# Kernel optimization log

Measured on AMD Instinct MI355X. Metric: run time of the kernel, lower is better.

## Reference

```python
import jax, jax.numpy as jnp
import numpy as np

SEQ_LEN = 2048
DIM = 1024
HEADS = 16
DIM_HEAD = 64
INNER = HEADS * DIM_HEAD
BASE = 10000.0


def rope_tables(seq_len, head_dim):
    inv_freq = 1.0 / (BASE ** (jnp.arange(0, head_dim, 2, dtype=jnp.float32) / head_dim))
    t = jnp.arange(seq_len, dtype=jnp.float32)
    freqs = jnp.einsum('i,j->ij', t, inv_freq)          # [n, d/2]
    emb = jnp.concatenate([freqs, freqs], axis=-1)       # [n, d]
    return jnp.cos(emb), jnp.sin(emb)                    # each [n, d]


def rotate_half(x):
    d = x.shape[-1] // 2
    return jnp.concatenate([-x[..., d:], x[..., :d]], axis=-1)


def setup_inputs() -> dict:
    key = jax.random.key(0)
    ks = jax.random.split(key, 5)
    x = jax.random.normal(ks[0], (2, SEQ_LEN, DIM), dtype=jnp.float32)
    W_qkv = jax.random.normal(ks[1], (DIM, 3 * INNER), dtype=jnp.float32) * (DIM ** -0.5)
    W_out = jax.random.normal(ks[2], (INNER, DIM), dtype=jnp.float32) * (INNER ** -0.5)
    b_out = jnp.zeros((DIM,), dtype=jnp.float32)
    ln_g = jnp.ones((DIM,), dtype=jnp.float32)
    ln_b = jnp.zeros((DIM,), dtype=jnp.float32)
    return {"x": x, "W_qkv": W_qkv, "W_out": W_out, "b_out": b_out, "ln_g": ln_g, "ln_b": ln_b}


def reference(x, W_qkv, W_out, b_out, ln_g, ln_b):
    b, n, _ = x.shape
    # LayerNorm
    mu = jnp.mean(x, axis=-1, keepdims=True)
    var = jnp.mean(jnp.square(x - mu), axis=-1, keepdims=True)
    xn = (x - mu) * jax.lax.rsqrt(var + 1e-5) * ln_g + ln_b
    # QKV projection -> [b, h, n, d]
    qkv = xn @ W_qkv                                   # [b, n, 3*inner]
    q, k, v = jnp.split(qkv, 3, axis=-1)
    def to_heads(t):
        return t.reshape(b, n, HEADS, DIM_HEAD).transpose(0, 2, 1, 3)
    q, k, v = to_heads(q), to_heads(k), to_heads(v)
    # RoPE
    cos, sin = rope_tables(n, DIM_HEAD)                # [n, d]
    cos = cos[None, None]                              # [1,1,n,d]
    sin = sin[None, None]
    q = q * cos + rotate_half(q) * sin
    k = k * cos + rotate_half(k) * sin
    # Attention
    scale = DIM_HEAD ** -0.5
    dots = jnp.einsum('bhid,bhjd->bhij', q, k) * scale  # [b,h,n,n]
    causal = jnp.tril(jnp.ones((n, n), dtype=bool))
    dots = jnp.where(causal[None, None], dots, jnp.float32(-jnp.inf))
    attn = jax.nn.softmax(dots, axis=-1)
    out = jnp.einsum('bhij,bhjd->bhid', attn, v)       # [b,h,n,d]
    out = out.transpose(0, 2, 1, 3).reshape(b, n, INNER)
    return out @ W_out + b_out
```

## Files before the change

kernel.cpp:

```cpp
#include <hip/hip_runtime.h>
#include <hip/hip_bf16.h>

#define SEQ    2048
#define DMODEL 1024
#define HEADS  16
#define DHEAD  64
#define BATCH  2
#define TOK    (BATCH * SEQ)
#define NQKV   (3 * DMODEL)
#define QK_SCALE (0.125f * 1.4426950408889634f)

typedef __attribute__((ext_vector_type(8))) short bf16x8;
typedef __attribute__((ext_vector_type(4))) float f32x4;

__device__ __forceinline__ float bf2f(ushort u) {
  union { unsigned int i; float f; } v; v.i = ((unsigned int)u) << 16; return v.f;
}
__device__ __forceinline__ ushort f2bf(float f) {
  union { float f; unsigned int i; } v; v.f = f;
  unsigned int r = (v.i + 0x7fffu + ((v.i >> 16) & 1u)) >> 16;
  return (ushort)r;
}

__device__ __forceinline__ int swz(int row, int byteoff) {
  return row * 128 + (byteoff ^ ((row & 7) << 4));
}
__device__ __forceinline__ int kperm(int s) {
  return (s & 0x20) | ((s & 0x0C) << 1) | ((s & 0x10) >> 2) | (s & 3);
}

#define GLL16(g, l)                                                                     \
  __builtin_amdgcn_global_load_lds((const __attribute__((address_space(1))) void*)(g),  \
                                   (__attribute__((address_space(3))) void*)(l), 16, 0, 0)

__global__ __launch_bounds__(256) void ln_kernel(const float* __restrict__ x,
                                                 const float* __restrict__ g,
                                                 const float* __restrict__ b,
                                                 ushort* __restrict__ xn) {
  int t = blockIdx.x;
  int tid = threadIdx.x;
  const float* row = x + (size_t)t * DMODEL;
  float4 v = *(const float4*)(row + tid * 4);
  float s  = v.x + v.y + v.z + v.w;
  float s2 = v.x * v.x + v.y * v.y + v.z * v.z + v.w * v.w;
#pragma unroll
  for (int m = 32; m >= 1; m >>= 1) {
    s  += __shfl_down(s, m);
    s2 += __shfl_down(s2, m);
  }
  __shared__ float ws[4], ws2[4];
  if ((tid & 63) == 0) { ws[tid >> 6] = s; ws2[tid >> 6] = s2; }
  __syncthreads();
  s  = ws[0] + ws[1] + ws[2] + ws[3];
  s2 = ws2[0] + ws2[1] + ws2[2] + ws2[3];
  float mu  = s * (1.f / DMODEL);
  float var = s2 * (1.f / DMODEL) - mu * mu;
  float rs  = rsqrtf(var + 1e-5f);
  float4 gv = *(const float4*)(g + tid * 4);
  float4 bv = *(const float4*)(b + tid * 4);
  ushort4 o;
  o.x = f2bf((v.x - mu) * rs * gv.x + bv.x);
  o.y = f2bf((v.y - mu) * rs * gv.y + bv.y);
  o.z = f2bf((v.z - mu) * rs * gv.z + bv.z);
  o.w = f2bf((v.w - mu) * rs * gv.w + bv.w);
  *(ushort4*)(xn + (size_t)t * DMODEL + tid * 4) = o;
}

__global__ void transpose_f2b(const float* __restrict__ in, ushort* __restrict__ out,
                              int R, int C) {
  __shared__ float tile[32][33];
  int c0 = blockIdx.x * 32, r0 = blockIdx.y * 32;
  int x = threadIdx.x, y = threadIdx.y;
#pragma unroll
  for (int i = 0; i < 32; i += 8) tile[y + i][x] = in[(size_t)(r0 + y + i) * C + c0 + x];
  __syncthreads();
#pragma unroll
  for (int i = 0; i < 32; i += 8) out[(size_t)(c0 + y + i) * R + r0 + x] = f2bf(tile[x][y + i]);
}

__global__ void rope_tab_kernel(float* __restrict__ ct, float* __restrict__ st) {
  int n = blockIdx.x, d = threadIdx.x;
  float invf = expf(-logf(10000.f) * (float)(d & 31) * (1.f / 32.f));
  float a = (float)n * invf;
  ct[n * DHEAD + d] = cosf(a);
  st[n * DHEAD + d] = sinf(a);
}

template<int EPI>
__global__ __launch_bounds__(256) void gemm_bt(const ushort* __restrict__ A,
                                               const ushort* __restrict__ BT,
                                               float* __restrict__ Cf,
                                               const float* __restrict__ bias,
                                               ushort* __restrict__ qh,
                                               ushort* __restrict__ kh,
                                               ushort* __restrict__ vh,
                                               const float* __restrict__ ct,
                                               const float* __restrict__ st,
                                               int M, int N, int K) {
  __shared__ __align__(16) ushort As[128 * 32];
  __shared__ __align__(16) ushort Bs[128 * 32];
  int tid = threadIdx.x;
  int w = tid >> 6, lane = tid & 63;
  int lrow = lane & 15, g = lane >> 4;
  int m0 = blockIdx.y * 128, n0 = blockIdx.x * 128;
  int wr = (w >> 1) * 64, wc = (w & 1) * 64;
  int grow = lane >> 2;
  int gcol = ((lane & 3) ^ ((grow >> 1) & 3)) * 8;
  ushort* ldsA0 = As + w * 512;
  ushort* ldsA1 = As + 2048 + w * 512;
  ushort* ldsB0 = Bs + w * 512;
  ushort* ldsB1 = Bs + 2048 + w * 512;
  int fcol = (g ^ ((lrow >> 1) & 3)) * 8;
  f32x4 acc[4][4] = {};
  for (int k0 = 0; k0 < K; k0 += 32) {
    __syncthreads();
    GLL16(A  + (size_t)(m0 + w * 16 + grow) * K + k0 + gcol, ldsA0);
    GLL16(A  + (size_t)(m0 + 64 + w * 16 + grow) * K + k0 + gcol, ldsA1);
    GLL16(BT + (size_t)(n0 + w * 16 + grow) * K + k0 + gcol, ldsB0);
    GLL16(BT + (size_t)(n0 + 64 + w * 16 + grow) * K + k0 + gcol, ldsB1);
    __syncthreads();
    bf16x8 af[4], bfr[4];
#pragma unroll
    for (int i = 0; i < 4; i++) af[i]  = *(const bf16x8*)(As + (wr + i * 16 + lrow) * 32 + fcol);
#pragma unroll
    for (int i = 0; i < 4; i++) bfr[i] = *(const bf16x8*)(Bs + (wc + i * 16 + lrow) * 32 + fcol);
    __builtin_amdgcn_s_setprio(1);
#pragma unroll
    for (int mf = 0; mf < 4; mf++)
#pragma unroll
      for (int nf = 0; nf < 4; nf++)
        acc[mf][nf] = __builtin_amdgcn_mfma_f32_16x16x32_bf16(af[mf], bfr[nf], acc[mf][nf], 0, 0, 0);
    __builtin_amdgcn_s_setprio(0);
  }
#pragma unroll
  for (int mf = 0; mf < 4; mf++)
#pragma unroll
    for (int nf = 0; nf < 4; nf++) {
      int col = n0 + wc + nf * 16 + lrow;
#pragma unroll
      for (int r = 0; r < 4; r++) {
        int rowi = m0 + wr + mf * 16 + g * 4 + r;
        float val = acc[mf][nf][r];
        if (EPI == 2) {
          Cf[(size_t)rowi * N + col] = val + bias[col];
        } else {
          int mat = col >> 10, c1 = col & 1023;
          int h = c1 >> 6, d = c1 & 63;
          int bb = rowi >> 11, n = rowi & (SEQ - 1);
          if (mat < 2) {
            float partner = acc[mf][nf ^ 2][r];
            float cs = ct[n * DHEAD + d], sn = st[n * DHEAD + d];
            float sgn = (d & 32) ? 1.f : -1.f;
            val = val * cs + sgn * partner * sn;
            if (mat == 0) val *= QK_SCALE;
          }
          ushort* dst = (mat == 0) ? qh : (mat == 1) ? kh : vh;
          dst[((size_t)(bb * HEADS + h) * SEQ + n) * DHEAD + d] = f2bf(val);
        }
      }
    }
}

__global__ __launch_bounds__(256) void attn_kernel(const ushort* __restrict__ q,
                                                   const ushort* __restrict__ k,
                                                   const ushort* __restrict__ v,
                                                   ushort* __restrict__ ao) {
  int wgid = blockIdx.x + gridDim.x * blockIdx.y;
  int j5 = wgid >> 3;
  int bh  = (wgid & 7) * 4 + (j5 >> 4);
  int pid = j5 & 15;
  int qlo = pid, qhi = (SEQ / 64 - 1) - pid;
  int tid = threadIdx.x, w = tid >> 6, lane = tid & 63;
  int lrow = lane & 15, g = lane >> 4;
  __shared__ __align__(16) ushort Ks[2][64 * 64];
  __shared__ __align__(16) ushort Vt[2][64 * 64];
  const ushort* qb = q + (size_t)bh * SEQ * DHEAD;
  const ushort* kb = k + (size_t)bh * SEQ * DHEAD;
  const ushort* vb = v + (size_t)bh * SEQ * DHEAD;
  const ushort* qph = qb + (size_t)(qhi * 64 + w * 16 + lrow) * DHEAD + g * 8;
  const ushort* qpl = qb + (size_t)(qlo * 64 + w * 16 + lrow) * DHEAD + g * 8;
  bf16x8 qh0 = *(const bf16x8*)(qph), qh1 = *(const bf16x8*)(qph + 32);
  bf16x8 ql0 = *(const bf16x8*)(qpl), ql1 = *(const bf16x8*)(qpl + 32);
  f32x4 aOh[4] = {}, aOl[4] = {};
  float l_hi = 0.f, l_lo = 0.f;

  int krow = tid >> 2, kco = (tid & 3) * 16;
  int pik = kperm(krow);
  int d0 = (tid & 31) * 2, kv8 = (tid >> 5) * 8;
  int4 ka0, ka1;
  unsigned int vd[8];

#define STAGE_ISSUE(j)                                                          \
  {                                                                             \
    const ushort* ks = kb + ((size_t)((j) * 64 + pik)) * DHEAD + kco;           \
    ka0 = *(const int4*)ks;                                                     \
    ka1 = *(const int4*)(ks + 8);                                               \
    const ushort* vs = vb + ((size_t)((j) * 64 + kv8)) * DHEAD + d0;            \
    _Pragma("unroll")                                                           \
    for (int jj = 0; jj < 8; jj++) vd[jj] = *(const unsigned int*)(vs + jj * DHEAD); \
  }

#define STAGE_WRITE(bsel)                                                       \
  {                                                                             \
    char* kd = (char*)Ks[bsel];                                                 \
    *(int4*)(kd + swz(krow, (tid & 3) * 32)) = ka0;                             \
    *(int4*)(kd + swz(krow, (tid & 3) * 32 + 16)) = ka1;                        \
    unsigned int lo[4], hi[4];                                                  \
    _Pragma("unroll")                                                           \
    for (int jj = 0; jj < 4; jj++) {                                            \
      lo[jj] = __builtin_amdgcn_perm(vd[2 * jj + 1], vd[2 * jj], 0x05040100u);  \
      hi[jj] = __builtin_amdgcn_perm(vd[2 * jj + 1], vd[2 * jj], 0x07060302u);  \
    }                                                                           \
    char* vdst = (char*)Vt[bsel];                                               \
    *(int4*)(vdst + swz(d0, kv8 * 2))     = *(int4*)lo;                         \
    *(int4*)(vdst + swz(d0 + 1, kv8 * 2)) = *(int4*)hi;                         \
  }

  STAGE_ISSUE(0);
  STAGE_WRITE(0);
  __syncthreads();
  int cur = 0;

  for (int jt = 0; jt <= qhi; jt++) {
    if (jt < qhi) STAGE_ISSUE(jt + 1);
    const char* kbuf = (const char*)Ks[cur];
    const char* vbuf = (const char*)Vt[cur];
    bf16x8 kf[8];
#pragma unroll
    for (int nf = 0; nf < 4; nf++) {
      kf[2 * nf]     = *(const bf16x8*)(kbuf + swz(nf * 16 + lrow, g * 16));
      kf[2 * nf + 1] = *(const bf16x8*)(kbuf + swz(nf * 16 + lrow, g * 16 + 64));
    }
    bf16x8 pah0, pah1, pal0, pal1;
    bool do_lo = (jt <= qlo);
    {
      f32x4 aS[4] = {};
      __builtin_amdgcn_s_setprio(1);
#pragma unroll
      for (int nf = 0; nf < 4; nf++) {
        aS[nf] = __builtin_amdgcn_mfma_f32_16x16x32_bf16(kf[2 * nf], qh0, aS[nf], 0, 0, 0);
        aS[nf] = __builtin_amdgcn_mfma_f32_16x16x32_bf16(kf[2 * nf + 1], qh1, aS[nf], 0, 0, 0);
      }
      __builtin_amdgcn_s_setprio(0);
      union { bf16x8 v; __hip_bfloat162 h[4]; } a0, a1;
      bool diag = (jt == qhi);
#pragma unroll
      for (int nf = 0; nf < 4; nf++) {
        float p[4];
#pragma unroll
        for (int r = 0; r < 4; r++) {
          int kvl = (nf >> 1) * 32 + g * 8 + (nf & 1) * 4 + r;
          p[r] = exp2f(aS[nf][r]);
          if (diag && kvl > w * 16 + lrow) p[r] = 0.f;
          l_hi += p[r];
        }
        __hip_bfloat162 plo = __float22bfloat162_rn({p[0], p[1]});
        __hip_bfloat162 phi = __float22bfloat162_rn({p[2], p[3]});
        if (nf < 2) { a0.h[(nf & 1) * 2] = plo; a0.h[(nf & 1) * 2 + 1] = phi; }
        else        { a1.h[(nf & 1) * 2] = plo; a1.h[(nf & 1) * 2 + 1] = phi; }
      }
      pah0 = a0.v; pah1 = a1.v;
    }
    if (do_lo) {
      f32x4 aS[4] = {};
      __builtin_amdgcn_s_setprio(1);
#pragma unroll
      for (int nf = 0; nf < 4; nf++) {
        aS[nf] = __builtin_amdgcn_mfma_f32_16x16x32_bf16(kf[2 * nf], ql0, aS[nf], 0, 0, 0);
        aS[nf] = __builtin_amdgcn_mfma_f32_16x16x32_bf16(kf[2 * nf + 1], ql1, aS[nf], 0, 0, 0);
      }
      __builtin_amdgcn_s_setprio(0);
      union { bf16x8 v; __hip_bfloat162 h[4]; } a0, a1;
      bool diag = (jt == qlo);
#pragma unroll
      for (int nf = 0; nf < 4; nf++) {
        float p[4];
#pragma unroll
        for (int r = 0; r < 4; r++) {
          int kvl = (nf >> 1) * 32 + g * 8 + (nf & 1) * 4 + r;
          p[r] = exp2f(aS[nf][r]);
          if (diag && kvl > w * 16 + lrow) p[r] = 0.f;
          l_lo += p[r];
        }
        __hip_bfloat162 plo = __float22bfloat162_rn({p[0], p[1]});
        __hip_bfloat162 phi = __float22bfloat162_rn({p[2], p[3]});
        if (nf < 2) { a0.h[(nf & 1) * 2] = plo; a0.h[(nf & 1) * 2 + 1] = phi; }
        else        { a1.h[(nf & 1) * 2] = plo; a1.h[(nf & 1) * 2 + 1] = phi; }
      }
      pal0 = a0.v; pal1 = a1.v;
    }
    bf16x8 vf[8];
#pragma unroll
    for (int nf = 0; nf < 4; nf++) {
      vf[2 * nf]     = *(const bf16x8*)(vbuf + swz(nf * 16 + lrow, g * 16));
      vf[2 * nf + 1] = *(const bf16x8*)(vbuf + swz(nf * 16 + lrow, g * 16 + 64));
    }
    __builtin_amdgcn_s_setprio(1);
#pragma unroll
    for (int nf = 0; nf < 4; nf++) {
      aOh[nf] = __builtin_amdgcn_mfma_f32_16x16x32_bf16(pah0, vf[2 * nf], aOh[nf], 0, 0, 0);
      aOh[nf] = __builtin_amdgcn_mfma_f32_16x16x32_bf16(pah1, vf[2 * nf + 1], aOh[nf], 0, 0, 0);
    }
    if (do_lo) {
#pragma unroll
      for (int nf = 0; nf < 4; nf++) {
        aOl[nf] = __builtin_amdgcn_mfma_f32_16x16x32_bf16(pal0, vf[2 * nf], aOl[nf], 0, 0, 0);
        aOl[nf] = __builtin_amdgcn_mfma_f32_16x16x32_bf16(pal1, vf[2 * nf + 1], aOl[nf], 0, 0, 0);
      }
    }
    __builtin_amdgcn_s_setprio(0);
    if (jt < qhi) STAGE_WRITE(cur ^ 1);
    __syncthreads();
    cur ^= 1;
  }

  l_hi += __shfl_xor(l_hi, 16); l_hi += __shfl_xor(l_hi, 32);
  l_lo += __shfl_xor(l_lo, 16); l_lo += __shfl_xor(l_lo, 32);
  int b = bh >> 4, h = bh & 15;
#pragma unroll
  for (int r = 0; r < 4; r++) {
    float ih = 1.f / __shfl(l_hi, g * 4 + r);
    float il = 1.f / __shfl(l_lo, g * 4 + r);
#pragma unroll
    for (int nf = 0; nf < 4; nf++) {
      int col = h * DHEAD + nf * 16 + lrow;
      int th = b * SEQ + qhi * 64 + w * 16 + g * 4 + r;
      int tl = b * SEQ + qlo * 64 + w * 16 + g * 4 + r;
      ao[(size_t)th * DMODEL + col] = f2bf(aOh[nf][r] * ih);
      ao[(size_t)tl * DMODEL + col] = f2bf(aOl[nf][r] * il);
    }
  }
#undef STAGE_ISSUE
#undef STAGE_WRITE
}

extern "C" void kernel_launch(void* const* d_in, const int* in_sizes, int n_in,
                              void* d_out, int out_size, void* d_ws, size_t ws_size,
                              hipStream_t stream) {
  const float* x    = (const float*)d_in[0];
  const float* Wqkv = (const float*)d_in[1];
  const float* Wout = (const float*)d_in[2];
  const float* bout = (const float*)d_in[3];
  const float* lng  = (const float*)d_in[4];
  const float* lnb  = (const float*)d_in[5];
  float* out = (float*)d_out;

  ushort* xn    = (ushort*)d_ws;
  ushort* WqkvT = xn + (size_t)TOK * DMODEL;
  ushort* WoutT = WqkvT + (size_t)NQKV * DMODEL;
  ushort* qh    = WoutT + (size_t)DMODEL * DMODEL;
  ushort* kh    = qh + (size_t)BATCH * HEADS * SEQ * DHEAD;
  ushort* vh    = kh + (size_t)BATCH * HEADS * SEQ * DHEAD;
  float*  ct    = (float*)(vh + (size_t)BATCH * HEADS * SEQ * DHEAD);
  float*  st    = ct + SEQ * DHEAD;
  ushort* ao    = xn;

  hipLaunchKernelGGL(ln_kernel, dim3(TOK), dim3(256), 0, stream, x, lng, lnb, xn);
  hipLaunchKernelGGL(transpose_f2b, dim3(NQKV / 32, DMODEL / 32), dim3(32, 8), 0, stream,
                     Wqkv, WqkvT, DMODEL, NQKV);
  hipLaunchKernelGGL(transpose_f2b, dim3(DMODEL / 32, DMODEL / 32), dim3(32, 8), 0, stream,
                     Wout, WoutT, DMODEL, DMODEL);
  hipLaunchKernelGGL(rope_tab_kernel, dim3(SEQ), dim3(DHEAD), 0, stream, ct, st);
  hipLaunchKernelGGL(gemm_bt<1>, dim3(NQKV / 128, TOK / 128), dim3(256), 0, stream,
                     xn, WqkvT, (float*)nullptr, (const float*)nullptr,
                     qh, kh, vh, ct, st, TOK, NQKV, DMODEL);
  hipLaunchKernelGGL(attn_kernel, dim3(16, BATCH * HEADS), dim3(256), 0, stream,
                     qh, kh, vh, ao);
  hipLaunchKernelGGL(gemm_bt<2>, dim3(DMODEL / 128, TOK / 128), dim3(256), 0, stream,
                     ao, WoutT, out, bout,
                     (ushort*)nullptr, (ushort*)nullptr, (ushort*)nullptr,
                     (const float*)nullptr, (const float*)nullptr, TOK, DMODEL, DMODEL);
}
```

Before: 135.3 us.

## Double-buffer LDS tiles in GEMM to overlap global loads with MFMA

Turns the single-buffered shared-memory A/B tiles in the bf16 GEMM into two ping-pong buffers. The next K-slice is issued via direct global-to-LDS loads while MFMAs run on the current one, with one barrier per step instead of two. This is meant to hide global load latency that the old load-sync-compute loop exposed. It doubles LDS use to 32KB per block, which can lower occupancy, and it assumes an even number of K steps.

```diff
diff --git a/kernel.cpp b/kernel.cpp
--- a/kernel.cpp
+++ b/kernel.cpp
@@ -97,8 +97,8 @@
                                                const float* __restrict__ ct,
                                                const float* __restrict__ st,
                                                int M, int N, int K) {
-  __shared__ __align__(16) ushort As[128 * 32];
-  __shared__ __align__(16) ushort Bs[128 * 32];
+  __shared__ __align__(16) ushort As[2][128 * 32];
+  __shared__ __align__(16) ushort Bs[2][128 * 32];
   int tid = threadIdx.x;
   int w = tid >> 6, lane = tid & 63;
   int lrow = lane & 15, g = lane >> 4;
@@ -106,32 +106,51 @@
   int wr = (w >> 1) * 64, wc = (w & 1) * 64;
   int grow = lane >> 2;
   int gcol = ((lane & 3) ^ ((grow >> 1) & 3)) * 8;
-  ushort* ldsA0 = As + w * 512;
-  ushort* ldsA1 = As + 2048 + w * 512;
-  ushort* ldsB0 = Bs + w * 512;
-  ushort* ldsB1 = Bs + 2048 + w * 512;
   int fcol = (g ^ ((lrow >> 1) & 3)) * 8;
+  const ushort* arow0 = A  + (size_t)(m0 + w * 16 + grow) * K + gcol;
+  const ushort* arow1 = A  + (size_t)(m0 + 64 + w * 16 + grow) * K + gcol;
+  const ushort* brow0 = BT + (size_t)(n0 + w * 16 + grow) * K + gcol;
+  const ushort* brow1 = BT + (size_t)(n0 + 64 + w * 16 + grow) * K + gcol;
   f32x4 acc[4][4] = {};
-  for (int k0 = 0; k0 < K; k0 += 32) {
+
+#define GSTAGE(bsel, k0)                              \
+  {                                                   \
+    GLL16(arow0 + (k0), As[bsel] + w * 512);          \
+    GLL16(arow1 + (k0), As[bsel] + 2048 + w * 512);   \
+    GLL16(brow0 + (k0), Bs[bsel] + w * 512);          \
+    GLL16(brow1 + (k0), Bs[bsel] + 2048 + w * 512);   \
+  }
+
+#define GCOMPUTE(bsel)                                                                     \
+  {                                                                                        \
+    bf16x8 af[4], bfr[4];                                                                  \
+    _Pragma("unroll")                                                                      \
+    for (int i = 0; i < 4; i++) af[i]  = *(const bf16x8*)(As[bsel] + (wr + i * 16 + lrow) * 32 + fcol); \
+    _Pragma("unroll")                                                                      \
+    for (int i = 0; i < 4; i++) bfr[i] = *(const bf16x8*)(Bs[bsel] + (wc + i * 16 + lrow) * 32 + fcol); \
+    __builtin_amdgcn_s_setprio(1);                                                         \
+    _Pragma("unroll")                                                                      \
+    for (int mf = 0; mf < 4; mf++)                                                         \
+      _Pragma("unroll")                                                                    \
+      for (int nf = 0; nf < 4; nf++)                                                       \
+        acc[mf][nf] = __builtin_amdgcn_mfma_f32_16x16x32_bf16(af[mf], bfr[nf], acc[mf][nf], 0, 0, 0); \
+    __builtin_amdgcn_s_setprio(0);                                                         \
+  }
+
+  int nk = K >> 5;
+  GSTAGE(0, 0);
+  __syncthreads();
+  for (int t = 0; t < nk; t += 2) {
+    if (t + 1 < nk) GSTAGE(1, (t + 1) << 5);
+    GCOMPUTE(0);
     __syncthreads();
-    GLL16(A  + (size_t)(m0 + w * 16 + grow) * K + k0 + gcol, ldsA0);
-    GLL16(A  + (size_t)(m0 + 64 + w * 16 + grow) * K + k0 + gcol, ldsA1);
-    GLL16(BT + (size_t)(n0 + w * 16 + grow) * K + k0 + gcol, ldsB0);
-    GLL16(BT + (size_t)(n0 + 64 + w * 16 + grow) * K + k0 + gcol, ldsB1);
+    if (t + 2 < nk) GSTAGE(0, (t + 2) << 5);
+    GCOMPUTE(1);
     __syncthreads();
-    bf16x8 af[4], bfr[4];
-#pragma unroll
-    for (int i = 0; i < 4; i++) af[i]  = *(const bf16x8*)(As + (wr + i * 16 + lrow) * 32 + fcol);
-#pragma unroll
-    for (int i = 0; i < 4; i++) bfr[i] = *(const bf16x8*)(Bs + (wc + i * 16 + lrow) * 32 + fcol);
-    __builtin_amdgcn_s_setprio(1);
-#pragma unroll
-    for (int mf = 0; mf < 4; mf++)
-#pragma unroll
-      for (int nf = 0; nf < 4; nf++)
-        acc[mf][nf] = __builtin_amdgcn_mfma_f32_16x16x32_bf16(af[mf], bfr[nf], acc[mf][nf], 0, 0, 0);
-    __builtin_amdgcn_s_setprio(0);
-  }
+  }
+#undef GSTAGE
+#undef GCOMPUTE
+
 #pragma unroll
   for (int mf = 0; mf < 4; mf++)
 #pragma unroll
```

After: 158.8 us. 1.17x slower.

## Replace paired causal q-tiles with one q-tile per block, longest-first order

Applied to the files above, without the earlier changes.

The attention kernel no longer pairs a low and a high query tile in each workgroup to balance causal work. It launches 1024 workgroups, one 64-row query tile each, ordered so the longest tiles (highest qt) are scheduled first, with heads spread across XCDs. This doubles block count for better occupancy and tail scheduling. In exchange each K/V tile loaded into LDS now serves only one query tile, so K/V traffic roughly doubles.

```diff
diff --git a/kernel.cpp b/kernel.cpp
--- a/kernel.cpp
+++ b/kernel.cpp
@@ -166,10 +166,9 @@
                                                    const ushort* __restrict__ v,
                                                    ushort* __restrict__ ao) {
   int wgid = blockIdx.x + gridDim.x * blockIdx.y;
-  int j5 = wgid >> 3;
-  int bh  = (wgid & 7) * 4 + (j5 >> 4);
-  int pid = j5 & 15;
-  int qlo = pid, qhi = (SEQ / 64 - 1) - pid;
+  int xcd = wgid & 7, idx = wgid >> 3;
+  int bh = xcd * 4 + (idx & 3);
+  int qt = 31 - (idx >> 2);
   int tid = threadIdx.x, w = tid >> 6, lane = tid & 63;
   int lrow = lane & 15, g = lane >> 4;
   __shared__ __align__(16) ushort Ks[2][64 * 64];
@@ -177,12 +176,10 @@
   const ushort* qb = q + (size_t)bh * SEQ * DHEAD;
   const ushort* kb = k + (size_t)bh * SEQ * DHEAD;
   const ushort* vb = v + (size_t)bh * SEQ * DHEAD;
-  const ushort* qph = qb + (size_t)(qhi * 64 + w * 16 + lrow) * DHEAD + g * 8;
-  const ushort* qpl = qb + (size_t)(qlo * 64 + w * 16 + lrow) * DHEAD + g * 8;
-  bf16x8 qh0 = *(const bf16x8*)(qph), qh1 = *(const bf16x8*)(qph + 32);
-  bf16x8 ql0 = *(const bf16x8*)(qpl), ql1 = *(const bf16x8*)(qpl + 32);
-  f32x4 aOh[4] = {}, aOl[4] = {};
-  float l_hi = 0.f, l_lo = 0.f;
+  const ushort* qp = qb + (size_t)(qt * 64 + w * 16 + lrow) * DHEAD + g * 8;
+  bf16x8 qf0 = *(const bf16x8*)(qp), qf1 = *(const bf16x8*)(qp + 32);
+  f32x4 aO[4] = {};
+  float l_s = 0.f;
 
   int krow = tid >> 2, kco = (tid & 3) * 16;
   int pik = kperm(krow);
@@ -221,8 +218,8 @@
   __syncthreads();
   int cur = 0;
 
-  for (int jt = 0; jt <= qhi; jt++) {
-    if (jt < qhi) STAGE_ISSUE(jt + 1);
+  for (int jt = 0; jt <= qt; jt++) {
+    if (jt < qt) STAGE_ISSUE(jt + 1);
     const char* kbuf = (const char*)Ks[cur];
     const char* vbuf = (const char*)Vt[cur];
     bf16x8 kf[8];
@@ -231,19 +228,18 @@
       kf[2 * nf]     = *(const bf16x8*)(kbuf + swz(nf * 16 + lrow, g * 16));
       kf[2 * nf + 1] = *(const bf16x8*)(kbuf + swz(nf * 16 + lrow, g * 16 + 64));
     }
-    bf16x8 pah0, pah1, pal0, pal1;
-    bool do_lo = (jt <= qlo);
+    bf16x8 pa0, pa1;
     {
       f32x4 aS[4] = {};
       __builtin_amdgcn_s_setprio(1);
 #pragma unroll
       for (int nf = 0; nf < 4; nf++) {
-        aS[nf] = __builtin_amdgcn_mfma_f32_16x16x32_bf16(kf[2 * nf], qh0, aS[nf], 0, 0, 0);
-        aS[nf] = __builtin_amdgcn_mfma_f32_16x16x32_bf16(kf[2 * nf + 1], qh1, aS[nf], 0, 0, 0);
+        aS[nf] = __builtin_amdgcn_mfma_f32_16x16x32_bf16(kf[2 * nf], qf0, aS[nf], 0, 0, 0);
+        aS[nf] = __builtin_amdgcn_mfma_f32_16x16x32_bf16(kf[2 * nf + 1], qf1, aS[nf], 0, 0, 0);
       }
       __builtin_amdgcn_s_setprio(0);
       union { bf16x8 v; __hip_bfloat162 h[4]; } a0, a1;
-      bool diag = (jt == qhi);
+      bool diag = (jt == qt);
 #pragma unroll
       for (int nf = 0; nf < 4; nf++) {
         float p[4];
@@ -252,42 +248,14 @@
           int kvl = (nf >> 1) * 32 + g * 8 + (nf & 1) * 4 + r;
           p[r] = exp2f(aS[nf][r]);
           if (diag && kvl > w * 16 + lrow) p[r] = 0.f;
-          l_hi += p[r];
+          l_s += p[r];
         }
         __hip_bfloat162 plo = __float22bfloat162_rn({p[0], p[1]});
         __hip_bfloat162 phi = __float22bfloat162_rn({p[2], p[3]});
         if (nf < 2) { a0.h[(nf & 1) * 2] = plo; a0.h[(nf & 1) * 2 + 1] = phi; }
         else        { a1.h[(nf & 1) * 2] = plo; a1.h[(nf & 1) * 2 + 1] = phi; }
       }
-      pah0 = a0.v; pah1 = a1.v;
-    }
-    if (do_lo) {
-      f32x4 aS[4] = {};
-      __builtin_amdgcn_s_setprio(1);
-#pragma unroll
-      for (int nf = 0; nf < 4; nf++) {
-        aS[nf] = __builtin_amdgcn_mfma_f32_16x16x32_bf16(kf[2 * nf], ql0, aS[nf], 0, 0, 0);
-        aS[nf] = __builtin_amdgcn_mfma_f32_16x16x32_bf16(kf[2 * nf + 1], ql1, aS[nf], 0, 0, 0);
-      }
-      __builtin_amdgcn_s_setprio(0);
-      union { bf16x8 v; __hip_bfloat162 h[4]; } a0, a1;
-      bool diag = (jt == qlo);
-#pragma unroll
-      for (int nf = 0; nf < 4; nf++) {
-        float p[4];
-#pragma unroll
-        for (int r = 0; r < 4; r++) {
-          int kvl = (nf >> 1) * 32 + g * 8 + (nf & 1) * 4 + r;
-          p[r] = exp2f(aS[nf][r]);
-          if (diag && kvl > w * 16 + lrow) p[r] = 0.f;
-          l_lo += p[r];
-        }
-        __hip_bfloat162 plo = __float22bfloat162_rn({p[0], p[1]});
-        __hip_bfloat162 phi = __float22bfloat162_rn({p[2], p[3]});
-        if (nf < 2) { a0.h[(nf & 1) * 2] = plo; a0.h[(nf & 1) * 2 + 1] = phi; }
-        else        { a1.h[(nf & 1) * 2] = plo; a1.h[(nf & 1) * 2 + 1] = phi; }
-      }
-      pal0 = a0.v; pal1 = a1.v;
+      pa0 = a0.v; pa1 = a1.v;
     }
     bf16x8 vf[8];
 #pragma unroll
@@ -298,36 +266,26 @@
     __builtin_amdgcn_s_setprio(1);
 #pragma unroll
     for (int nf = 0; nf < 4; nf++) {
-      aOh[nf] = __builtin_amdgcn_mfma_f32_16x16x32_bf16(pah0, vf[2 * nf], aOh[nf], 0, 0, 0);
-      aOh[nf] = __builtin_amdgcn_mfma_f32_16x16x32_bf16(pah1, vf[2 * nf + 1], aOh[nf], 0, 0, 0);
-    }
-    if (do_lo) {
-#pragma unroll
-      for (int nf = 0; nf < 4; nf++) {
-        aOl[nf] = __builtin_amdgcn_mfma_f32_16x16x32_bf16(pal0, vf[2 * nf], aOl[nf], 0, 0, 0);
-        aOl[nf] = __builtin_amdgcn_mfma_f32_16x16x32_bf16(pal1, vf[2 * nf + 1], aOl[nf], 0, 0, 0);
-      }
+      aO[nf] = __builtin_amdgcn_mfma_f32_16x16x32_bf16(pa0, vf[2 * nf], aO[nf], 0, 0, 0);
+      aO[nf] = __builtin_amdgcn_mfma_f32_16x16x32_bf16(pa1, vf[2 * nf + 1], aO[nf], 0, 0, 0);
     }
     __builtin_amdgcn_s_setprio(0);
-    if (jt < qhi) STAGE_WRITE(cur ^ 1);
+    if (jt < qt) STAGE_WRITE(cur ^ 1);
     __syncthreads();
     cur ^= 1;
   }
 
-  l_hi += __shfl_xor(l_hi, 16); l_hi += __shfl_xor(l_hi, 32);
-  l_lo += __shfl_xor(l_lo, 16); l_lo += __shfl_xor(l_lo, 32);
+  l_s += __shfl_xor(l_s, 16);
+  l_s += __shfl_xor(l_s, 32);
   int b = bh >> 4, h = bh & 15;
 #pragma unroll
   for (int r = 0; r < 4; r++) {
-    float ih = 1.f / __shfl(l_hi, g * 4 + r);
-    float il = 1.f / __shfl(l_lo, g * 4 + r);
+    float inv = 1.f / __shfl(l_s, g * 4 + r);
 #pragma unroll
     for (int nf = 0; nf < 4; nf++) {
       int col = h * DHEAD + nf * 16 + lrow;
-      int th = b * SEQ + qhi * 64 + w * 16 + g * 4 + r;
-      int tl = b * SEQ + qlo * 64 + w * 16 + g * 4 + r;
-      ao[(size_t)th * DMODEL + col] = f2bf(aOh[nf][r] * ih);
-      ao[(size_t)tl * DMODEL + col] = f2bf(aOl[nf][r] * il);
+      int tok = b * SEQ + qt * 64 + w * 16 + g * 4 + r;
+      ao[(size_t)tok * DMODEL + col] = f2bf(aO[nf][r] * inv);
     }
   }
 #undef STAGE_ISSUE
@@ -364,7 +322,7 @@
   hipLaunchKernelGGL(gemm_bt<1>, dim3(NQKV / 128, TOK / 128), dim3(256), 0, stream,
                      xn, WqkvT, (float*)nullptr, (const float*)nullptr,
                      qh, kh, vh, ct, st, TOK, NQKV, DMODEL);
-  hipLaunchKernelGGL(attn_kernel, dim3(16, BATCH * HEADS), dim3(256), 0, stream,
+  hipLaunchKernelGGL(attn_kernel, dim3(32, 32), dim3(256), 0, stream,
                      qh, kh, vh, ao);
   hipLaunchKernelGGL(gemm_bt<2>, dim3(DMODEL / 128, TOK / 128), dim3(256), 0, stream,
                      ao, WoutT, out, bout,
```

New measurement: 131.8 us. 1.03x faster.
